# Performance work log

Measured on AMD Instinct MI355X. Metric: run time of the kernel, lower is better.

The kernel has to match this reference:

```python
import jax, jax.numpy as jnp
import numpy as np

D_MODEL = 1024
NUM_HEADS = 16
D_HEAD = D_MODEL // NUM_HEADS
BATCH, SEQ, MEM = 2, 1024, 1024
TOT = SEQ + MEM


def setup_inputs() -> dict:
    key = jax.random.key(0)
    ks = jax.random.split(key, 16)
    s = 0.02
    return {
        "x": jax.random.normal(ks[0], (BATCH, SEQ, D_MODEL), jnp.float32),
        "mem": jax.random.normal(ks[1], (BATCH, MEM, D_MODEL), jnp.float32),
        "mask": jnp.zeros((1, 1, SEQ, TOT), jnp.float32),
        "rel_enc": jax.random.normal(ks[2], (TOT, D_MODEL), jnp.float32),
        "Wq": jax.random.normal(ks[3], (D_MODEL, D_MODEL), jnp.float32) * s,
        "bq": jnp.zeros((D_MODEL,), jnp.float32),
        "Wke": jax.random.normal(ks[4], (D_MODEL, D_MODEL), jnp.float32) * s,
        "bke": jnp.zeros((D_MODEL,), jnp.float32),
        "Wkr": jax.random.normal(ks[5], (D_MODEL, D_MODEL), jnp.float32) * s,
        "bkr": jnp.zeros((D_MODEL,), jnp.float32),
        "Wv": jax.random.normal(ks[6], (D_MODEL, D_MODEL), jnp.float32) * s,
        "bv": jnp.zeros((D_MODEL,), jnp.float32),
        "Wo": jax.random.normal(ks[7], (D_MODEL, D_MODEL), jnp.float32) * s,
        "bo": jnp.zeros((D_MODEL,), jnp.float32),
    }


def _split_heads(t, b):
    # (b, s, d_model) -> (b, h, s, d_head)
    return t.reshape(b, -1, NUM_HEADS, D_HEAD).transpose(0, 2, 1, 3)


def _rel_enc_shift(arr):
    # arr: (b, h, l, m) -> Transformer-XL shift trick
    b, h, l, m = arr.shape
    arr = jnp.concatenate([arr, jnp.zeros((b, h, l, 1), arr.dtype)], axis=-1)
    arr = arr.reshape(b, h, l * (m + 1))
    return arr[:, :, l - 1:-1].reshape(b, h, l, m)


def reference(x, mem, mask, rel_enc, Wq, bq, Wke, bke, Wkr, bkr, Wv, bv, Wo, bo):
    b, s, _ = x.shape
    x_tilde = jnp.concatenate([mem, x], axis=1)  # (b, tot, d)
    q = _split_heads(x @ Wq + bq, b)             # (b, h, s, dh)
    k = _split_heads(x_tilde @ Wke + bke, b)     # (b, h, tot, dh)
    v = _split_heads(x_tilde @ Wv + bv, b)       # (b, h, tot, dh)
    A = jnp.einsum("bhsd,bhtd->bhst", q, k)      # content scores
    Q = (rel_enc @ Wkr + bkr).reshape(-1, NUM_HEADS, D_HEAD).transpose(1, 0, 2)  # (h, tot, dh)
    B_hat = jnp.einsum("bhsd,htd->bhst", q, Q)
    B = _rel_enc_shift(B_hat)                    # relative-position scores
    scores = (A + B) / jnp.sqrt(jnp.float32(D_HEAD)) + mask * -1e9
    w = jax.nn.softmax(scores, axis=-1)
    out = jnp.einsum("bhst,bhtd->bhsd", w, v)
    out = out.transpose(0, 2, 1, 3).reshape(b, s, D_MODEL)
    return out @ Wo + bo
```

## Files before the change

kernel.cpp:

```cpp
#include <hip/hip_runtime.h>

typedef unsigned short ushort;
typedef unsigned int uint;
typedef __attribute__((ext_vector_type(8))) short short8;
typedef __attribute__((ext_vector_type(4))) float float4v;

#define D_MODEL 1024
#define NH 16
#define DH 64
#define BATCH 2
#define SEQ 1024
#define MEMLEN 1024
#define TOT 2048

__device__ __forceinline__ float b2f(ushort u) {
  return __uint_as_float(((uint)u) << 16);
}
__device__ __forceinline__ ushort f2b(float f) {
  uint i = __float_as_uint(f);
  uint r = (i + 0x7fffu + ((i >> 16) & 1u)) >> 16;
  return (ushort)r;
}
__device__ __forceinline__ void gld16(const ushort* g, ushort* l) {
  __builtin_amdgcn_global_load_lds(
      (const __attribute__((address_space(1))) void*)g,
      (__attribute__((address_space(3))) void*)l, 16, 0, 0);
}

__global__ __launch_bounds__(256) void concat_cvt_kernel(
    const float* __restrict__ x, const float* __restrict__ mem,
    ushort* __restrict__ xt, ushort* __restrict__ xb) {
  int idx = blockIdx.x * 256 + threadIdx.x;
  int row = idx >> 7;
  int c8 = (idx & 127) << 3;
  int b = row >> 11;
  int i = row & 2047;
  const float* src = (i < MEMLEN) ? &mem[((b << 10) + i) * D_MODEL]
                                  : &x[((b << 10) + (i - MEMLEN)) * D_MODEL];
  float4 f0 = *(const float4*)(&src[c8]);
  float4 f1 = *(const float4*)(&src[c8 + 4]);
  ushort u[8] = {f2b(f0.x), f2b(f0.y), f2b(f0.z), f2b(f0.w),
                 f2b(f1.x), f2b(f1.y), f2b(f1.z), f2b(f1.w)};
  *(uint4*)(&xt[row * D_MODEL + c8]) = *(const uint4*)u;
  if (i >= MEMLEN)
    *(uint4*)(&xb[((b << 10) + (i - MEMLEN)) * D_MODEL + c8]) = *(const uint4*)u;
}

__global__ __launch_bounds__(256) void cvt_kernel(const float* __restrict__ in,
                                                  ushort* __restrict__ out) {
  int idx = blockIdx.x * 256 + threadIdx.x;
  int base = idx << 3;
  float4 f0 = *(const float4*)(&in[base]);
  float4 f1 = *(const float4*)(&in[base + 4]);
  ushort u[8] = {f2b(f0.x), f2b(f0.y), f2b(f0.z), f2b(f0.w),
                 f2b(f1.x), f2b(f1.y), f2b(f1.z), f2b(f1.w)};
  *(uint4*)(&out[base]) = *(const uint4*)u;
}

__global__ __launch_bounds__(256) void maskcvt_kernel(
    const float* __restrict__ in, ushort* __restrict__ out) {
  int idx = blockIdx.x * 256 + threadIdx.x;
  int base = idx << 3;
  float4 f0 = *(const float4*)(&in[base]);
  float4 f1 = *(const float4*)(&in[base + 4]);
  ushort u[8] = {f2b(f0.x * -1e9f), f2b(f0.y * -1e9f), f2b(f0.z * -1e9f),
                 f2b(f0.w * -1e9f), f2b(f1.x * -1e9f), f2b(f1.y * -1e9f),
                 f2b(f1.z * -1e9f), f2b(f1.w * -1e9f)};
  *(uint4*)(&out[base]) = *(const uint4*)u;
}

__global__ __launch_bounds__(256) void transpose_cvt5_kernel(
    const float* __restrict__ W0, const float* __restrict__ W1,
    const float* __restrict__ W2, const float* __restrict__ W3,
    const float* __restrict__ W4, ushort* __restrict__ T0,
    ushort* __restrict__ T1, ushort* __restrict__ T2, ushort* __restrict__ T3,
    ushort* __restrict__ T4) {
  __shared__ ushort tle[32][33];
  const float* W;
  ushort* T;
  switch (blockIdx.z) {
    case 0: W = W0; T = T0; break;
    case 1: W = W1; T = T1; break;
    case 2: W = W2; T = T2; break;
    case 3: W = W3; T = T3; break;
    default: W = W4; T = T4; break;
  }
  const int bx = blockIdx.x * 32, by = blockIdx.y * 32;
  const int tx = threadIdx.x & 31, ty = threadIdx.x >> 5;
#pragma unroll
  for (int j = 0; j < 32; j += 8)
    tle[ty + j][tx] = f2b(W[(by + ty + j) * 1024 + bx + tx]);
  __syncthreads();
#pragma unroll
  for (int j = 0; j < 32; j += 8)
    T[(bx + ty + j) * 1024 + by + tx] = tle[tx][ty + j];
}

__global__ __launch_bounds__(256) void vtrans_kernel(
    const ushort* __restrict__ kv, ushort* __restrict__ vt) {
  __shared__ ushort tle[32][76];
  const int gx = blockIdx.x;
  const int gy = blockIdx.y;
  const int tid = threadIdx.x;
  const int r = tid >> 3, c8 = (tid & 7) * 8;
  *(uint4*)(&tle[r][c8]) =
      *(const uint4*)(&kv[(gx * 32 + r) * 2048 + 1024 + gy * 64 + c8]);
  __syncthreads();
  const int dr = tid >> 2, tc8 = (tid & 3) * 8;
  const int bb = (gx * 32) >> 11, tbase = (gx * 32) & 2047;
  ushort tmp[8];
#pragma unroll
  for (int j = 0; j < 8; ++j) tmp[j] = tle[tc8 + j][dr];
  *(uint4*)(&vt[((bb << 10) + gy * 64 + dr) * 2048 + tbase + tc8]) =
      *(const uint4*)tmp;
}

__global__ __launch_bounds__(256) void gemm128_kernel(
    const ushort* __restrict__ A, const ushort* __restrict__ BT,
    const float* __restrict__ b0, const float* __restrict__ b1,
    ushort* __restrict__ Cout, int M, int N, int K) {
  __shared__ ushort As[128 * 32];
  __shared__ ushort Bs[128 * 32];
  const int m0 = blockIdx.x * 128, n0 = blockIdx.y * 128;
  const int tid = threadIdx.x;
  const int w = tid >> 6, lane = tid & 63, m15 = lane & 15, q4 = lane >> 4;
  const int wm = w & 1, wn = w >> 1;
  float4v acc[4][4] = {};
  const int c0 = tid, c1 = tid + 256;
  const int r0 = c0 >> 2, u0 = (c0 & 3) * 8;
  const int r1 = c1 >> 2, u1 = (c1 & 3) * 8;

  for (int kk = 0; kk < K; kk += 32) {
    __syncthreads();
    gld16(&A[(m0 + r0) * K + kk + u0], &As[c0 * 8]);
    gld16(&A[(m0 + r1) * K + kk + u1], &As[c1 * 8]);
    gld16(&BT[(n0 + r0) * K + kk + u0], &Bs[c0 * 8]);
    gld16(&BT[(n0 + r1) * K + kk + u1], &Bs[c1 * 8]);
    __syncthreads();
    short8 af[4], bf[4];
#pragma unroll
    for (int i = 0; i < 4; ++i)
      af[i] = *(const short8*)(&As[(wm * 64 + i * 16 + m15) * 32 + q4 * 8]);
#pragma unroll
    for (int j = 0; j < 4; ++j)
      bf[j] = *(const short8*)(&Bs[(wn * 64 + j * 16 + m15) * 32 + q4 * 8]);
#pragma unroll
    for (int i = 0; i < 4; ++i)
#pragma unroll
      for (int j = 0; j < 4; ++j)
        acc[i][j] =
            __builtin_amdgcn_mfma_f32_16x16x32_bf16(af[i], bf[j], acc[i][j], 0, 0, 0);
  }
#pragma unroll
  for (int j = 0; j < 4; ++j) {
    int col = n0 + wn * 64 + j * 16 + m15;
    float bv = (col < 1024) ? b0[col] : b1[col - 1024];
    float sc = (col < 1024) ? 0.125f : 1.0f;
#pragma unroll
    for (int i = 0; i < 4; ++i) {
      int rowb = m0 + wm * 64 + i * 16 + q4 * 4;
#pragma unroll
      for (int r = 0; r < 4; ++r)
        Cout[(rowb + r) * N + col] = f2b((acc[i][j][r] + bv) * sc);
    }
  }
}

template <int EPI>
__global__ __launch_bounds__(256) void gemm64_kernel(
    const ushort* __restrict__ A, const ushort* __restrict__ BT0,
    const ushort* __restrict__ BT1, int rowSplit, const float* __restrict__ b0,
    const float* __restrict__ b1, float sc1, void* __restrict__ Cout, int M,
    int N, int K) {
  __shared__ ushort As[64 * 32];
  __shared__ ushort Bs[128 * 32];
  const int m0 = blockIdx.x * 64, n0 = blockIdx.y * 128;
  const ushort* BT = (m0 < rowSplit) ? BT0 : BT1;
  const float* bias = (m0 < rowSplit) ? b0 : b1;
  const float sc = (m0 < rowSplit) ? 1.0f : sc1;
  const int tid = threadIdx.x;
  const int w = tid >> 6, lane = tid & 63, m15 = lane & 15, q4 = lane >> 4;
  float4v acc[4][2] = {};
  const int ra = tid >> 2, ua = (tid & 3) * 8;
  const int c0 = tid, c1 = tid + 256;
  const int rb0 = c0 >> 2, ub0 = (c0 & 3) * 8;
  const int rb1 = c1 >> 2, ub1 = (c1 & 3) * 8;

  for (int kk = 0; kk < K; kk += 32) {
    __syncthreads();
    gld16(&A[(m0 + ra) * K + kk + ua], &As[tid * 8]);
    gld16(&BT[(n0 + rb0) * K + kk + ub0], &Bs[c0 * 8]);
    gld16(&BT[(n0 + rb1) * K + kk + ub1], &Bs[c1 * 8]);
    __syncthreads();
    short8 bf[2];
#pragma unroll
    for (int j = 0; j < 2; ++j)
      bf[j] = *(const short8*)(&Bs[(w * 32 + j * 16 + m15) * 32 + q4 * 8]);
#pragma unroll
    for (int i = 0; i < 4; ++i) {
      short8 af = *(const short8*)(&As[(i * 16 + m15) * 32 + q4 * 8]);
#pragma unroll
      for (int j = 0; j < 2; ++j)
        acc[i][j] =
            __builtin_amdgcn_mfma_f32_16x16x32_bf16(af, bf[j], acc[i][j], 0, 0, 0);
    }
  }
#pragma unroll
  for (int j = 0; j < 2; ++j) {
    int col = n0 + w * 32 + j * 16 + m15;
    float bv = bias[col];
#pragma unroll
    for (int i = 0; i < 4; ++i) {
      int rowb = m0 + i * 16 + q4 * 4;
#pragma unroll
      for (int r = 0; r < 4; ++r) {
        float v = (acc[i][j][r] + bv) * sc;
        if (EPI == 1)
          ((float*)Cout)[(rowb + r) * N + col] = v;
        else
          ((ushort*)Cout)[(rowb + r) * N + col] = f2b(v);
      }
    }
  }
}

__global__ __launch_bounds__(256) void bhat_kernel(
    const ushort* __restrict__ q, const ushort* __restrict__ Qrb,
    const ushort* __restrict__ maskb, ushort* __restrict__ Bh) {
  __shared__ ushort As[2 * 128 * 32];
  __shared__ ushort Bs[2 * 128 * 32];
  const int bs0 = blockIdx.x * 128, u0 = blockIdx.y * 128, h = blockIdx.z;
  const int tid = threadIdx.x;
  const int w = tid >> 6, lane = tid & 63, m15 = lane & 15, q4 = lane >> 4;
  const int wm = w & 1, wn = w >> 1;

#pragma unroll
  for (int c = 0; c < 4; ++c) {
    int unit = c * 256 + tid;
    int row = (unit >> 2) & 127, kh = unit >> 9, cu = unit & 3;
    gld16(&q[(bs0 + row) * 1024 + (h << 6) + kh * 32 + cu * 8], &As[unit * 8]);
    gld16(&Qrb[(u0 + row) * 1024 + (h << 6) + kh * 32 + cu * 8], &Bs[unit * 8]);
  }
  __syncthreads();

  float4v acc[4][4] = {};
#pragma unroll
  for (int kh = 0; kh < 2; ++kh) {
    short8 af[4], bf[4];
#pragma unroll
    for (int i = 0; i < 4; ++i)
      af[i] = *(const short8*)(&As[kh * 4096 + (wm * 64 + i * 16 + m15) * 32 + q4 * 8]);
#pragma unroll
    for (int j = 0; j < 4; ++j)
      bf[j] = *(const short8*)(&Bs[kh * 4096 + (wn * 64 + j * 16 + m15) * 32 + q4 * 8]);
#pragma unroll
    for (int i = 0; i < 4; ++i)
#pragma unroll
      for (int j = 0; j < 4; ++j)
        acc[i][j] =
            __builtin_amdgcn_mfma_f32_16x16x32_bf16(af[i], bf[j], acc[i][j], 0, 0, 0);
  }
  const int b = bs0 >> 10;
  const int s0loc = bs0 & 1023;
  const int outrow0 = ((b << 4) + h) * 1024 + s0loc;
#pragma unroll
  for (int j = 0; j < 4; ++j) {
    int u = u0 + wn * 64 + j * 16 + m15;
#pragma unroll
    for (int i = 0; i < 4; ++i) {
      int rowb = outrow0 + wm * 64 + i * 16 + q4 * 4;
      int spb = s0loc + wm * 64 + i * 16 + q4 * 4;
#pragma unroll
      for (int r = 0; r < 4; ++r) {
        int sp = spb + r;
        bool selA = (u >= 1023 - sp);
        int mrow = selA ? sp : (sp > 0 ? sp - 1 : 0);
        int mcol = selA ? (u + sp - 1023) : (u + sp + 1025);
        float mval = b2f(maskb[mrow * 2048 + mcol]);
        Bh[(rowb + r) * 2048 + u] = f2b(acc[i][j][r] + mval);
      }
    }
  }
}

__global__ __launch_bounds__(256) void attn_kernel(
    const ushort* __restrict__ qb, const ushort* __restrict__ kv,
    const ushort* __restrict__ vt, const ushort* __restrict__ Bh,
    const ushort* __restrict__ maskb, ushort* __restrict__ attn) {
  __shared__ ushort Pp[4][16 * 36];
  __shared__ float comb[2][16][68];
  __shared__ float csum[32];

  const int tid = threadIdx.x;
  const int w = tid >> 6, lane = tid & 63, m15 = lane & 15, q4 = lane >> 4;
  const int st = w & 1, th = w >> 1;
  const int s0w = blockIdx.x * 32 + st * 16;
  const int h = blockIdx.y, b = blockIdx.z;
  const int s_l = q4 * 4;

  const ushort* qp = &qb[((b << 10) + s0w + m15) * 1024 + (h << 6) + q4 * 8];
  const short8 af0 = *(const short8*)qp;
  const short8 af1 = *(const short8*)(qp + 32);

  const ushort* kvb = &kv[((size_t)(b << 11) * 2048) + (h << 6)];
  const ushort* vtb = &vt[((size_t)((b << 10) + (h << 6))) * 2048];
  const int bhbase = ((b << 4) + h) << 21;
  ushort* pw = &Pp[w][0];

  int offA[4], offB[4], diagT[4];
  float dm[4];
#pragma unroll
  for (int i = 0; i < 4; ++i) {
    int s = s0w + s_l + i;
    offA[i] = bhbase + (s << 11) - s + 1023;
    offB[i] = bhbase + ((s + 1) << 11) - s - 1026;
    diagT[i] = s + 1025;
    dm[i] = (diagT[i] <= 2047) ? b2f(maskb[s * 2048 + diagT[i]]) : 0.f;
  }

  float lsum4[4] = {0.f, 0.f, 0.f, 0.f};
  float4v oacc[4] = {};
  ushort Bb0[8], Bb1[8], Bb2[8], Bb3[8];

  auto pre_bh = [&](int t0, ushort (&B)[8]) {
#pragma unroll
    for (int nt = 0; nt < 2; ++nt)
#pragma unroll
      for (int i = 0; i < 4; ++i) {
        int t = t0 + nt * 16 + m15;
        int off = (t < diagT[i]) ? offA[i] : offB[i];
        B[nt * 4 + i] = Bh[off + t];
      }
  };

  auto phase = [&](int t0, ushort (&Bb)[8], bool pf) {
    short8 Vr[4], Kr[2][2];
#pragma unroll
    for (int nd = 0; nd < 4; ++nd)
      Vr[nd] = *(const short8*)(&vtb[(size_t)(nd * 16 + m15) * 2048 + t0 + q4 * 8]);
#pragma unroll
    for (int nt = 0; nt < 2; ++nt) {
      const ushort* kp = &kvb[(size_t)(t0 + nt * 16 + m15) * 2048 + q4 * 8];
      Kr[nt][0] = *(const short8*)kp;
      Kr[nt][1] = *(const short8*)(kp + 32);
    }
    ushort cur[8];
#pragma unroll
    for (int j = 0; j < 8; ++j) cur[j] = Bb[j];
    if (pf) pre_bh(t0 + 128, Bb);
    float4v a0 = {}, a1 = {};
    a0 = __builtin_amdgcn_mfma_f32_16x16x32_bf16(af0, Kr[0][0], a0, 0, 0, 0);
    a0 = __builtin_amdgcn_mfma_f32_16x16x32_bf16(af1, Kr[0][1], a0, 0, 0, 0);
    a1 = __builtin_amdgcn_mfma_f32_16x16x32_bf16(af0, Kr[1][0], a1, 0, 0, 0);
    a1 = __builtin_amdgcn_mfma_f32_16x16x32_bf16(af1, Kr[1][1], a1, 0, 0, 0);
#pragma unroll
    for (int nt = 0; nt < 2; ++nt)
#pragma unroll
      for (int i = 0; i < 4; ++i) {
        int t = t0 + nt * 16 + m15;
        float bv = (t == diagT[i]) ? dm[i] : b2f(cur[nt * 4 + i]);
        float a = (nt == 0) ? a0[i] : a1[i];
        float p = __expf(a + bv);
        lsum4[i] += p;
        pw[(s_l + i) * 36 + nt * 16 + m15] = f2b(p);
      }
    short8 pfr = *(const short8*)(&pw[m15 * 36 + q4 * 8]);
#pragma unroll
    for (int nd = 0; nd < 4; ++nd)
      oacc[nd] =
          __builtin_amdgcn_mfma_f32_16x16x32_bf16(pfr, Vr[nd], oacc[nd], 0, 0, 0);
  };

  const int tb = th * 1024;
  pre_bh(tb, Bb0);
  pre_bh(tb + 32, Bb1);
  pre_bh(tb + 64, Bb2);
  pre_bh(tb + 96, Bb3);
  for (int it = 0; it < 8; ++it) {
    const int t0 = tb + it * 128;
    const bool pf = (it < 7);
    phase(t0, Bb0, pf);
    phase(t0 + 32, Bb1, pf);
    phase(t0 + 64, Bb2, pf);
    phase(t0 + 96, Bb3, pf);
  }

#pragma unroll
  for (int i = 0; i < 4; ++i) {
    float v = lsum4[i];
    v += __shfl_xor(v, 1, 64);
    v += __shfl_xor(v, 2, 64);
    v += __shfl_xor(v, 4, 64);
    v += __shfl_xor(v, 8, 64);
    lsum4[i] = v;
  }
  if (th == 1) {
#pragma unroll
    for (int nd = 0; nd < 4; ++nd)
#pragma unroll
      for (int i = 0; i < 4; ++i)
        comb[st][s_l + i][nd * 16 + m15] = oacc[nd][i];
    if (m15 == 0)
#pragma unroll
      for (int i = 0; i < 4; ++i) csum[st * 16 + s_l + i] = lsum4[i];
  }
  __syncthreads();
  if (th == 0) {
#pragma unroll
    for (int i = 0; i < 4; ++i) lsum4[i] += csum[st * 16 + s_l + i];
#pragma unroll
    for (int nd = 0; nd < 4; ++nd)
#pragma unroll
      for (int i = 0; i < 4; ++i) {
        float v = oacc[nd][i] + comb[st][s_l + i][nd * 16 + m15];
        attn[((b << 10) + s0w + s_l + i) * 1024 + (h << 6) + nd * 16 + m15] =
            f2b(v / lsum4[i]);
      }
  }
}

extern "C" void kernel_launch(void* const* d_in, const int* in_sizes, int n_in,
                              void* d_out, int out_size, void* d_ws,
                              size_t ws_size, hipStream_t stream) {
  const float* x = (const float*)d_in[0];
  const float* mem = (const float*)d_in[1];
  const float* mask = (const float*)d_in[2];
  const float* rel = (const float*)d_in[3];
  const float* Wq = (const float*)d_in[4];
  const float* bq = (const float*)d_in[5];
  const float* Wke = (const float*)d_in[6];
  const float* bke = (const float*)d_in[7];
  const float* Wkr = (const float*)d_in[8];
  const float* bkr = (const float*)d_in[9];
  const float* Wv = (const float*)d_in[10];
  const float* bv = (const float*)d_in[11];
  const float* Wo = (const float*)d_in[12];
  const float* bo = (const float*)d_in[13];
  float* out = (float*)d_out;

  ushort* ws = (ushort*)d_ws;
  ushort* xt = ws;
  ushort* xbrel = xt + 4096 * 1024;
  ushort* WqT = xbrel + 4096 * 1024;
  ushort* WkeT = WqT + 1024 * 1024;
  ushort* WvT = WkeT + 1024 * 1024;
  ushort* WkrT = WvT + 1024 * 1024;
  ushort* WoT = WkrT + 1024 * 1024;
  ushort* kv = WoT + 1024 * 1024;
  ushort* qr = kv + 4096 * 2048;
  ushort* attn = qr + 4096 * 1024;
  ushort* maskb = attn + 2048 * 1024;
  ushort* Bh = maskb + 1024 * 2048;
  ushort* relb = xbrel + 2048 * 1024;
  ushort* Qrb = qr + 2048 * 1024;
  ushort* vt = xt;

  concat_cvt_kernel<<<2048, 256, 0, stream>>>(x, mem, xt, xbrel);
  cvt_kernel<<<1024, 256, 0, stream>>>(rel, relb);
  maskcvt_kernel<<<1024, 256, 0, stream>>>(mask, maskb);
  transpose_cvt5_kernel<<<dim3(32, 32, 5), 256, 0, stream>>>(
      Wq, Wke, Wkr, Wv, Wo, WqT, WkeT, WkrT, WvT, WoT);

  gemm128_kernel<<<dim3(32, 16), 256, 0, stream>>>(xt, WkeT, bke, bv, kv,
                                                   4096, 2048, 1024);
  gemm64_kernel<0><<<dim3(64, 8), 256, 0, stream>>>(
      xbrel, WqT, WkrT, 2048, bq, bkr, 0.125f, qr, 4096, 1024, 1024);
  vtrans_kernel<<<dim3(128, 16), 256, 0, stream>>>(kv, vt);

  bhat_kernel<<<dim3(16, 16, 16), 256, 0, stream>>>(qr, Qrb, maskb, Bh);

  attn_kernel<<<dim3(SEQ / 32, NH, BATCH), 256, 0, stream>>>(
      qr, kv, vt, Bh, maskb, attn);

  gemm64_kernel<1><<<dim3(32, 8), 256, 0, stream>>>(
      attn, WoT, WoT, 1 << 30, bo, bo, 1.0f, out, 2048, 1024, 1024);
}
```

Before: 371.6 us.

## Fuse KV and Q/Kr projection GEMMs; split attention key range across four waves

```diff
diff --git a/kernel.cpp b/kernel.cpp
--- a/kernel.cpp
+++ b/kernel.cpp
@@ -115,13 +115,37 @@
       *(const uint4*)tmp;
 }
 
-__global__ __launch_bounds__(256) void gemm128_kernel(
-    const ushort* __restrict__ A, const ushort* __restrict__ BT,
-    const float* __restrict__ b0, const float* __restrict__ b1,
-    ushort* __restrict__ Cout, int M, int N, int K) {
+__global__ __launch_bounds__(256) void gemm_fused_kernel(
+    const ushort* __restrict__ xt, const ushort* __restrict__ xbrel,
+    const ushort* __restrict__ WkeT, const ushort* __restrict__ WqT,
+    const ushort* __restrict__ WkrT, const float* __restrict__ bke,
+    const float* __restrict__ bv, const float* __restrict__ bq,
+    const float* __restrict__ bkr, ushort* __restrict__ kv,
+    ushort* __restrict__ qr) {
   __shared__ ushort As[128 * 32];
   __shared__ ushort Bs[128 * 32];
-  const int m0 = blockIdx.x * 128, n0 = blockIdx.y * 128;
+  const int bid = blockIdx.x;
+  const bool seg0 = (bid < 512);
+  const ushort* A;
+  const ushort* BT;
+  ushort* C;
+  int ldC, m0, n0;
+  if (seg0) {
+    m0 = (bid & 31) * 128;
+    n0 = (bid >> 5) * 128;
+    A = xt;
+    BT = WkeT;
+    C = kv;
+    ldC = 2048;
+  } else {
+    int g = bid - 512;
+    m0 = (g & 31) * 128;
+    n0 = (g >> 5) * 128;
+    A = xbrel;
+    BT = (m0 < 2048) ? WqT : WkrT;
+    C = qr;
+    ldC = 1024;
+  }
   const int tid = threadIdx.x;
   const int w = tid >> 6, lane = tid & 63, m15 = lane & 15, q4 = lane >> 4;
   const int wm = w & 1, wn = w >> 1;
@@ -130,12 +154,12 @@
   const int r0 = c0 >> 2, u0 = (c0 & 3) * 8;
   const int r1 = c1 >> 2, u1 = (c1 & 3) * 8;
 
-  for (int kk = 0; kk < K; kk += 32) {
+  for (int kk = 0; kk < 1024; kk += 32) {
     __syncthreads();
-    gld16(&A[(m0 + r0) * K + kk + u0], &As[c0 * 8]);
-    gld16(&A[(m0 + r1) * K + kk + u1], &As[c1 * 8]);
-    gld16(&BT[(n0 + r0) * K + kk + u0], &Bs[c0 * 8]);
-    gld16(&BT[(n0 + r1) * K + kk + u1], &Bs[c1 * 8]);
+    gld16(&A[(m0 + r0) * 1024 + kk + u0], &As[c0 * 8]);
+    gld16(&A[(m0 + r1) * 1024 + kk + u1], &As[c1 * 8]);
+    gld16(&BT[(n0 + r0) * 1024 + kk + u0], &Bs[c0 * 8]);
+    gld16(&BT[(n0 + r1) * 1024 + kk + u1], &Bs[c1 * 8]);
     __syncthreads();
     short8 af[4], bf[4];
 #pragma unroll
@@ -154,30 +178,32 @@
 #pragma unroll
   for (int j = 0; j < 4; ++j) {
     int col = n0 + wn * 64 + j * 16 + m15;
-    float bv = (col < 1024) ? b0[col] : b1[col - 1024];
-    float sc = (col < 1024) ? 0.125f : 1.0f;
+    float bb, sc;
+    if (seg0) {
+      bb = (col < 1024) ? bke[col] : bv[col - 1024];
+      sc = (col < 1024) ? 0.125f : 1.0f;
+    } else {
+      bb = (m0 < 2048) ? bq[col] : bkr[col];
+      sc = (m0 < 2048) ? 1.0f : 0.125f;
+    }
 #pragma unroll
     for (int i = 0; i < 4; ++i) {
       int rowb = m0 + wm * 64 + i * 16 + q4 * 4;
 #pragma unroll
       for (int r = 0; r < 4; ++r)
-        Cout[(rowb + r) * N + col] = f2b((acc[i][j][r] + bv) * sc);
+        C[(rowb + r) * ldC + col] = f2b((acc[i][j][r] + bb) * sc);
     }
   }
 }
 
 template <int EPI>
 __global__ __launch_bounds__(256) void gemm64_kernel(
-    const ushort* __restrict__ A, const ushort* __restrict__ BT0,
-    const ushort* __restrict__ BT1, int rowSplit, const float* __restrict__ b0,
-    const float* __restrict__ b1, float sc1, void* __restrict__ Cout, int M,
-    int N, int K) {
+    const ushort* __restrict__ A, const ushort* __restrict__ BT,
+    const float* __restrict__ bias, void* __restrict__ Cout, int M, int N,
+    int K) {
   __shared__ ushort As[64 * 32];
   __shared__ ushort Bs[128 * 32];
   const int m0 = blockIdx.x * 64, n0 = blockIdx.y * 128;
-  const ushort* BT = (m0 < rowSplit) ? BT0 : BT1;
-  const float* bias = (m0 < rowSplit) ? b0 : b1;
-  const float sc = (m0 < rowSplit) ? 1.0f : sc1;
   const int tid = threadIdx.x;
   const int w = tid >> 6, lane = tid & 63, m15 = lane & 15, q4 = lane >> 4;
   float4v acc[4][2] = {};
@@ -214,7 +240,7 @@
       int rowb = m0 + i * 16 + q4 * 4;
 #pragma unroll
       for (int r = 0; r < 4; ++r) {
-        float v = (acc[i][j][r] + bv) * sc;
+        float v = acc[i][j][r] + bv;
         if (EPI == 1)
           ((float*)Cout)[(rowb + r) * N + col] = v;
         else
@@ -288,13 +314,13 @@
     const ushort* __restrict__ vt, const ushort* __restrict__ Bh,
     const ushort* __restrict__ maskb, ushort* __restrict__ attn) {
   __shared__ ushort Pp[4][16 * 36];
-  __shared__ float comb[2][16][68];
-  __shared__ float csum[32];
+  __shared__ float comb[3][16][68];
+  __shared__ float csum[3][16];
 
   const int tid = threadIdx.x;
   const int w = tid >> 6, lane = tid & 63, m15 = lane & 15, q4 = lane >> 4;
-  const int st = w & 1, th = w >> 1;
-  const int s0w = blockIdx.x * 32 + st * 16;
+  const int th = w;
+  const int s0w = blockIdx.x * 16;
   const int h = blockIdx.y, b = blockIdx.z;
   const int s_l = q4 * 4;
 
@@ -371,14 +397,14 @@
           __builtin_amdgcn_mfma_f32_16x16x32_bf16(pfr, Vr[nd], oacc[nd], 0, 0, 0);
   };
 
-  const int tb = th * 1024;
+  const int tb = th * 512;
   pre_bh(tb, Bb0);
   pre_bh(tb + 32, Bb1);
   pre_bh(tb + 64, Bb2);
   pre_bh(tb + 96, Bb3);
-  for (int it = 0; it < 8; ++it) {
+  for (int it = 0; it < 4; ++it) {
     const int t0 = tb + it * 128;
-    const bool pf = (it < 7);
+    const bool pf = (it < 3);
     phase(t0, Bb0, pf);
     phase(t0 + 32, Bb1, pf);
     phase(t0 + 64, Bb2, pf);
@@ -394,25 +420,28 @@
     v += __shfl_xor(v, 8, 64);
     lsum4[i] = v;
   }
-  if (th == 1) {
+  if (th > 0) {
 #pragma unroll
     for (int nd = 0; nd < 4; ++nd)
 #pragma unroll
       for (int i = 0; i < 4; ++i)
-        comb[st][s_l + i][nd * 16 + m15] = oacc[nd][i];
+        comb[th - 1][s_l + i][nd * 16 + m15] = oacc[nd][i];
     if (m15 == 0)
 #pragma unroll
-      for (int i = 0; i < 4; ++i) csum[st * 16 + s_l + i] = lsum4[i];
+      for (int i = 0; i < 4; ++i) csum[th - 1][s_l + i] = lsum4[i];
   }
   __syncthreads();
   if (th == 0) {
 #pragma unroll
-    for (int i = 0; i < 4; ++i) lsum4[i] += csum[st * 16 + s_l + i];
+    for (int i = 0; i < 4; ++i)
+      lsum4[i] += csum[0][s_l + i] + csum[1][s_l + i] + csum[2][s_l + i];
 #pragma unroll
     for (int nd = 0; nd < 4; ++nd)
 #pragma unroll
       for (int i = 0; i < 4; ++i) {
-        float v = oacc[nd][i] + comb[st][s_l + i][nd * 16 + m15];
+        float v = oacc[nd][i] + comb[0][s_l + i][nd * 16 + m15] +
+                  comb[1][s_l + i][nd * 16 + m15] +
+                  comb[2][s_l + i][nd * 16 + m15];
         attn[((b << 10) + s0w + s_l + i) * 1024 + (h << 6) + nd * 16 + m15] =
             f2b(v / lsum4[i]);
       }
@@ -461,17 +490,15 @@
   transpose_cvt5_kernel<<<dim3(32, 32, 5), 256, 0, stream>>>(
       Wq, Wke, Wkr, Wv, Wo, WqT, WkeT, WkrT, WvT, WoT);
 
-  gemm128_kernel<<<dim3(32, 16), 256, 0, stream>>>(xt, WkeT, bke, bv, kv,
-                                                   4096, 2048, 1024);
-  gemm64_kernel<0><<<dim3(64, 8), 256, 0, stream>>>(
-      xbrel, WqT, WkrT, 2048, bq, bkr, 0.125f, qr, 4096, 1024, 1024);
+  gemm_fused_kernel<<<768, 256, 0, stream>>>(xt, xbrel, WkeT, WqT, WkrT, bke,
+                                             bv, bq, bkr, kv, qr);
   vtrans_kernel<<<dim3(128, 16), 256, 0, stream>>>(kv, vt);
 
   bhat_kernel<<<dim3(16, 16, 16), 256, 0, stream>>>(qr, Qrb, maskb, Bh);
 
-  attn_kernel<<<dim3(SEQ / 32, NH, BATCH), 256, 0, stream>>>(
+  attn_kernel<<<dim3(SEQ / 16, NH, BATCH), 256, 0, stream>>>(
       qr, kv, vt, Bh, maskb, attn);
 
-  gemm64_kernel<1><<<dim3(32, 8), 256, 0, stream>>>(
-      attn, WoT, WoT, 1 << 30, bo, bo, 1.0f, out, 2048, 1024, 1024);
-}
+  gemm64_kernel<1><<<dim3(32, 8), 256, 0, stream>>>(attn, WoT, bo, out, 2048,
+                                                    1024, 1024);
+}
```

Result: no change. 373.0 us (+0.4%).
